# Optimization experiments

Measured on AMD Instinct MI355X. Metric: run time of the kernel, lower is better.

Reference implementation:

```python
import jax, jax.numpy as jnp
import numpy as np

B, S, D = 4, 4096, 768

def setup_inputs() -> dict:
    key = jax.random.key(0)
    kx, kq, kk, kv = jax.random.split(key, 4)
    x = jax.random.normal(kx, (B, S, D), dtype=jnp.float32)
    Wq = jax.random.normal(kq, (D, D), dtype=jnp.float32) * (D ** -0.5)
    Wk = jax.random.normal(kk, (D, D), dtype=jnp.float32) * (D ** -0.5)
    Wv = jax.random.normal(kv, (D, D), dtype=jnp.float32) * (D ** -0.5)
    return {"x": x, "Wq": Wq, "Wk": Wk, "Wv": Wv}

def reference(x, Wq, Wk, Wv):
    # q,k,v: [B,S,D]  (Linear with no bias)
    q = x @ Wq
    k = x @ Wk
    v = x @ Wv
    # full N x N causal score matrix, as in the original module
    scores = jnp.einsum('bqd,bkd->bqk', q, k)  # [B,S,S]
    seq = scores.shape[1]
    causal_mask = jnp.triu(jnp.ones((seq, seq), dtype=bool), k=1)  # True above diagonal
    scores = jnp.where(causal_mask[None, :, :], -jnp.inf, scores)
    scale = jnp.asarray(k.shape[-1], scores.dtype) ** 0.5
    weights = jax.nn.softmax(scores / scale, axis=-1)  # [B,S,S]
    # dropout p=0.0 -> identity (deterministic reference)
    context = jnp.einsum('bqk,bkd->bqd', weights, v)  # [B,S,D]
    return context
```

## Files before the change

### kernel.cpp

```cpp
#include <hip/hip_runtime.h>
#include <hip/hip_bf16.h>

typedef __attribute__((ext_vector_type(8))) _Float16 half8_t;
typedef __attribute__((ext_vector_type(4))) _Float16 half4_t;
typedef __attribute__((ext_vector_type(4))) float float4_t;

#define D_DIM 768
#define S_DIM 4096
#define B_DIM 4
#define M_DIM (B_DIM * S_DIM)
#define SD ((size_t)S_DIM * D_DIM)

#define GLOAD_LDS16(g, s)                                      \
  __builtin_amdgcn_global_load_lds(                            \
      (const __attribute__((address_space(1))) void*)(g),      \
      (__attribute__((address_space(3))) void*)(s), 16, 0, 0)

__device__ __forceinline__ float4_t mfma16(half8_t a, half8_t b, float4_t c) {
  return __builtin_amdgcn_mfma_f32_16x16x32_f16(a, b, c, 0, 0, 0);
}

__global__ __launch_bounds__(256) void prep_kernel(const float* __restrict__ x,
                                                   const float* __restrict__ W0,
                                                   const float* __restrict__ W1,
                                                   const float* __restrict__ W2,
                                                   _Float16* __restrict__ xh,
                                                   _Float16* __restrict__ WT) {
  __shared__ _Float16 tile[64][68];
  const int bid = blockIdx.x;
  if (bid < 12288) {
    int i = (bid * 256 + threadIdx.x) * 4;
    float4 v = *(const float4*)(x + i);
    half4_t o;
    o.x = (_Float16)v.x; o.y = (_Float16)v.y; o.z = (_Float16)v.z; o.w = (_Float16)v.w;
    *(half4_t*)(xh + i) = o;
  } else {
    int t = bid - 12288;
    int z = t / 144;
    int r = t % 144;
    int kx = r / 12, ny = r % 12;
    const float* W = (z == 0) ? W0 : (z == 1) ? W1 : W2;
    _Float16* o = WT + (size_t)z * D_DIM * D_DIM;
    int k0 = kx * 64, n0 = ny * 64;
#pragma unroll
    for (int i = 0; i < 16; ++i) {
      int idx = threadIdx.x + i * 256;
      int rr = idx >> 6, cc = idx & 63;
      tile[rr][cc] = (_Float16)W[(size_t)(k0 + rr) * D_DIM + n0 + cc];
    }
    __syncthreads();
#pragma unroll
    for (int i = 0; i < 16; ++i) {
      int idx = threadIdx.x + i * 256;
      int rr = idx >> 6, cc = idx & 63;
      o[(size_t)(n0 + rr) * D_DIM + k0 + cc] = tile[cc][rr];
    }
  }
}

template <bool SWAP>
__device__ __forceinline__ void core128(const _Float16* __restrict__ Ag,
                                        const _Float16* __restrict__ Bg,
                                        int lda, int ldb, int nt,
                                        char* lds, float4_t (&acc)[4][4]) {
  const int tid = threadIdx.x;
  const int w = tid >> 6, l = tid & 63;
  const int wr = w >> 1, wc = w & 1;
  const int l15 = l & 15, l4 = l >> 4;

  int sA[4], sB[4], sDst[4];
#pragma unroll
  for (int i = 0; i < 4; ++i) {
    int L = i * 256 + tid;
    int row = L >> 3, u = L & 7;
    int usw = u ^ (row & 7);
    sA[i] = row * lda + usw * 8;
    sB[i] = row * ldb + usw * 8;
    sDst[i] = (i * 256 + (tid & ~63)) * 16;
  }

  int aOff[2][4], bOff[2][4];
#pragma unroll
  for (int ks = 0; ks < 2; ++ks) {
#pragma unroll
    for (int i = 0; i < 4; ++i) {
      int ar = wr * 64 + i * 16 + l15;
      aOff[ks][i] = ar * 128 + (((ks * 4 + l4) ^ (ar & 7)) * 16);
      int br = wc * 64 + i * 16 + l15;
      bOff[ks][i] = 16384 + br * 128 + (((ks * 4 + l4) ^ (br & 7)) * 16);
    }
  }

#pragma unroll 1
  for (int kt = 0; kt < nt; ++kt) {
#pragma unroll
    for (int i = 0; i < 4; ++i)
      GLOAD_LDS16(Ag + (size_t)kt * 64 + sA[i], lds + sDst[i]);
#pragma unroll
    for (int i = 0; i < 4; ++i)
      GLOAD_LDS16(Bg + (size_t)kt * 64 + sB[i], lds + 16384 + sDst[i]);
    __syncthreads();
#pragma unroll
    for (int ks = 0; ks < 2; ++ks) {
      half8_t af[4], bf[4];
#pragma unroll
      for (int ni = 0; ni < 4; ++ni) bf[ni] = *(const half8_t*)(lds + bOff[ks][ni]);
#pragma unroll
      for (int mi = 0; mi < 4; ++mi) af[mi] = *(const half8_t*)(lds + aOff[ks][mi]);
      __builtin_amdgcn_s_setprio(1);
#pragma unroll
      for (int mi = 0; mi < 4; ++mi)
#pragma unroll
        for (int ni = 0; ni < 4; ++ni) {
          if (SWAP)
            acc[mi][ni] = mfma16(bf[ni], af[mi], acc[mi][ni]);
          else
            acc[mi][ni] = mfma16(af[mi], bf[ni], acc[mi][ni]);
        }
      __builtin_amdgcn_s_setprio(0);
    }
    __syncthreads();
  }
}

__global__ __launch_bounds__(256) void proj8_kernel(const _Float16* __restrict__ xh,
                                                    const _Float16* __restrict__ WT,
                                                    _Float16* __restrict__ qkv,
                                                    _Float16* __restrict__ vt) {
  __shared__ __align__(16) char lds[32768];
  const int bid = blockIdx.x;
  const int wid = (bid & 7) * 288 + (bid >> 3);
  const int rbg = wid / 18;
  const int rem = wid % 18;
  const int z = rem / 6;
  const int cb = rem % 6;

  const _Float16* Ag = xh + (size_t)rbg * 128 * D_DIM;
  const _Float16* Bg = WT + (size_t)z * D_DIM * D_DIM + (size_t)cb * 128 * D_DIM;
  float4_t acc[4][4];
#pragma unroll
  for (int a = 0; a < 4; ++a)
#pragma unroll
    for (int b = 0; b < 4; ++b) acc[a][b] = (float4_t){0.f, 0.f, 0.f, 0.f};

  const int tid = threadIdx.x;
  const int w = tid >> 6, l = tid & 63;
  const int wr = w >> 1, wc = w & 1;
  const int l15 = l & 15, l4 = l >> 4;

  if (z < 2) {
    core128<false>(Ag, Bg, D_DIM, D_DIM, 12, lds, acc);
    _Float16* C = qkv + (size_t)z * M_DIM * D_DIM;
#pragma unroll
    for (int mi = 0; mi < 4; ++mi)
#pragma unroll
      for (int ni = 0; ni < 4; ++ni) {
        int col = cb * 128 + wc * 64 + ni * 16 + l15;
#pragma unroll
        for (int j = 0; j < 4; ++j) {
          int row = rbg * 128 + wr * 64 + mi * 16 + l4 * 4 + j;
          C[(size_t)row * D_DIM + col] = (_Float16)acc[mi][ni][j];
        }
      }
  } else {
    core128<true>(Ag, Bg, D_DIM, D_DIM, 12, lds, acc);
#pragma unroll
    for (int mi = 0; mi < 4; ++mi) {
      int scol = rbg * 128 + wr * 64 + mi * 16 + l15;
      int bb = scol >> 12;
      int sl = scol & 4095;
      _Float16* vtb = vt + (size_t)bb * SD;
#pragma unroll
      for (int ni = 0; ni < 4; ++ni) {
#pragma unroll
        for (int j = 0; j < 4; ++j) {
          int drow = cb * 128 + wc * 64 + ni * 16 + l4 * 4 + j;
          vtb[(size_t)drow * S_DIM + sl] = (_Float16)acc[mi][ni][j];
        }
      }
    }
  }
}

__global__ __launch_bounds__(256) void gemm1_8_kernel(const _Float16* __restrict__ Q,
                                                      const _Float16* __restrict__ K,
                                                      _Float16* __restrict__ P,
                                                      float* __restrict__ rp) {
  __shared__ __align__(16) char lds[32768];
  const float SCALE = 0.036084391824351615f;
  const int bid = blockIdx.x;
  const int wid = (bid & 7) * 264 + (bid >> 3);
  const int z = wid / 528;
  const int t = wid % 528;
  int g = 0;
  while (g < 7 && (8 * (g + 1) * g + 10 * (g + 1)) <= t) ++g;
  int r = t - (8 * g * (g - 1) + 10 * g);
  int rbg, cb;
  if (r < 16 * g) {
    int cbg = r >> 4, wi = r & 15;
    rbg = 4 * g + (wi >> 2);
    cb = 4 * cbg + (wi & 3);
  } else {
    int r2 = r - 16 * g;
    const int ri[10] = {0, 1, 1, 2, 2, 2, 3, 3, 3, 3};
    const int rj[10] = {0, 0, 1, 0, 1, 2, 0, 1, 2, 3};
    rbg = 4 * g + ri[r2];
    cb = 4 * g + rj[r2];
  }

  const _Float16* Ag = Q + (size_t)z * SD + (size_t)rbg * 128 * D_DIM;
  const _Float16* Bg = K + (size_t)z * SD + (size_t)cb * 128 * D_DIM;
  float4_t acc[4][4];
#pragma unroll
  for (int a = 0; a < 4; ++a)
#pragma unroll
    for (int b = 0; b < 4; ++b) acc[a][b] = (float4_t){0.f, 0.f, 0.f, 0.f};
  core128<false>(Ag, Bg, D_DIM, D_DIM, 12, lds, acc);

  const int tid = threadIdx.x;
  const int w = tid >> 6, l = tid & 63;
  const int wr = w >> 1, wc = w & 1;
  const int l15 = l & 15, l4 = l >> 4;
  _Float16* Pz = P + (size_t)z * S_DIM * S_DIM;
  float* rpz = rp + (size_t)z * S_DIM * 64;
#pragma unroll
  for (int mi = 0; mi < 4; ++mi) {
#pragma unroll
    for (int j = 0; j < 4; ++j) {
      int row = rbg * 128 + wr * 64 + mi * 16 + l4 * 4 + j;
      float rs = 0.f;
#pragma unroll
      for (int ni = 0; ni < 4; ++ni) {
        int col = cb * 128 + wc * 64 + ni * 16 + l15;
        float v = (col <= row) ? __expf(acc[mi][ni][j] * SCALE - 4.0f) : 0.f;
        _Float16 ph = (_Float16)v;
        Pz[(size_t)row * S_DIM + col] = ph;
        rs += (float)ph;
      }
#pragma unroll
      for (int d = 1; d < 16; d <<= 1) rs += __shfl_xor(rs, d);
      if (l15 == 0) rpz[(size_t)row * 64 + cb * 2 + wc] = rs;
    }
  }
}

__global__ __launch_bounds__(256) void gemm2_8_kernel(const _Float16* __restrict__ P,
                                                      const _Float16* __restrict__ VT,
                                                      float* __restrict__ outp,
                                                      const float* __restrict__ rp) {
  __shared__ __align__(16) char lds[32768];
  __shared__ float rsm[128];
  const int bid = blockIdx.x;
  const int g = bid / 24;
  const int q = bid % 24;
  const int rbg = 31 - g;
  const int xcd = q & 7;
  const int slot = q >> 3;
  const int z = xcd >> 1;
  const int by = (xcd & 1) * 3 + slot;
  const int nt = 2 * (rbg + 1);

  const _Float16* Ag = P + (size_t)z * S_DIM * S_DIM + (size_t)rbg * 128 * S_DIM;
  const _Float16* Bg = VT + (size_t)z * SD + (size_t)by * 128 * S_DIM;
  float4_t acc[4][4];
#pragma unroll
  for (int a = 0; a < 4; ++a)
#pragma unroll
    for (int b = 0; b < 4; ++b) acc[a][b] = (float4_t){0.f, 0.f, 0.f, 0.f};
  core128<false>(Ag, Bg, S_DIM, S_DIM, nt, lds, acc);

  const int tid = threadIdx.x;
  if (tid < 128) {
    const float* p = rp + ((size_t)z * S_DIM + (size_t)rbg * 128 + tid) * 64;
    float s = 0.f;
    for (int i = 0; i < nt; ++i) s += p[i];
    rsm[tid] = 1.0f / s;
  }
  __syncthreads();

  const int w = tid >> 6, l = tid & 63;
  const int wr = w >> 1, wc = w & 1;
  const int l15 = l & 15, l4 = l >> 4;
#pragma unroll
  for (int mi = 0; mi < 4; ++mi) {
#pragma unroll
    for (int j = 0; j < 4; ++j) {
      int lrow = wr * 64 + mi * 16 + l4 * 4 + j;
      int row = rbg * 128 + lrow;
      float rinv = rsm[lrow];
#pragma unroll
      for (int ni = 0; ni < 4; ++ni) {
        int col = by * 128 + wc * 64 + ni * 16 + l15;
        outp[(size_t)z * SD + (size_t)row * D_DIM + col] = acc[mi][ni][j] * rinv;
      }
    }
  }
}

extern "C" void kernel_launch(void* const* d_in, const int* in_sizes, int n_in,
                              void* d_out, int out_size, void* d_ws, size_t ws_size,
                              hipStream_t stream) {
  const float* x = (const float*)d_in[0];
  const float* Wq = (const float*)d_in[1];
  const float* Wk = (const float*)d_in[2];
  const float* Wv = (const float*)d_in[3];
  float* out = (float*)d_out;
  char* ws = (char*)d_ws;

  const size_t XH_B = (size_t)M_DIM * D_DIM * 2;
  const size_t QKV_B = 3 * XH_B;
  const size_t VT_B = XH_B;
  const size_t WT_B = (size_t)3 * D_DIM * D_DIM * 2;
  const size_t BASE_END = XH_B + QKV_B + VT_B + WT_B;

  _Float16* xh = (_Float16*)ws;
  _Float16* qkv = (_Float16*)(ws + XH_B);
  _Float16* Q = qkv;
  _Float16* K = qkv + (size_t)M_DIM * D_DIM;
  _Float16* vt = (_Float16*)(ws + XH_B + QKV_B);
  _Float16* wt = (_Float16*)(ws + XH_B + QKV_B + VT_B);

  float* rp = (float*)(ws + BASE_END);
  _Float16* P = (_Float16*)(ws + BASE_END + (size_t)4259840);

  prep_kernel<<<dim3(12720), dim3(256), 0, stream>>>(x, Wq, Wk, Wv, xh, wt);
  proj8_kernel<<<dim3(2304), dim3(256), 0, stream>>>(xh, wt, qkv, vt);
  gemm1_8_kernel<<<dim3(2112), dim3(256), 0, stream>>>(Q, K, P, rp);
  gemm2_8_kernel<<<dim3(768), dim3(256), 0, stream>>>(P, vt, out, rp);
}
```

Measured before the change: 264.4 us.

## Double-buffer GEMM core with async LDS prefetch and 32-wide K tiles

The shared GEMM core now uses two 16KB LDS buffers with K-tiles of 32 instead of one 32KB buffer with K-tiles of 64. The next tile is prefetched via global_load_lds while the current one feeds MFMAs, synchronized with explicit vmcnt waits and raw barriers. This is meant to hide global-load latency behind compute. The cost is twice as many iterations and barriers, each doing half the MFMA work, plus a new swizzle for the narrower rows. Callers' tile counts are doubled, and the row-sum loop keeps its old count.

```diff
diff --git a/kernel.cpp b/kernel.cpp
--- a/kernel.cpp
+++ b/kernel.cpp
@@ -68,59 +68,71 @@
   const int wr = w >> 1, wc = w & 1;
   const int l15 = l & 15, l4 = l >> 4;
 
-  int sA[4], sB[4], sDst[4];
+  int aS[2], bS[2], dstL[2];
+#pragma unroll
+  for (int i = 0; i < 2; ++i) {
+    int g = i * 256 + tid;
+    int row = g >> 2, u = g & 3;
+    int usw = (u ^ ((row >> 1) & 3)) * 8;
+    aS[i] = row * lda + usw;
+    bS[i] = row * ldb + usw;
+    dstL[i] = (i * 256 + (tid & ~63)) * 16;
+  }
+
+  int aOff[4], bOff[4];
 #pragma unroll
   for (int i = 0; i < 4; ++i) {
-    int L = i * 256 + tid;
-    int row = L >> 3, u = L & 7;
-    int usw = u ^ (row & 7);
-    sA[i] = row * lda + usw * 8;
-    sB[i] = row * ldb + usw * 8;
-    sDst[i] = (i * 256 + (tid & ~63)) * 16;
-  }
-
-  int aOff[2][4], bOff[2][4];
-#pragma unroll
-  for (int ks = 0; ks < 2; ++ks) {
-#pragma unroll
-    for (int i = 0; i < 4; ++i) {
-      int ar = wr * 64 + i * 16 + l15;
-      aOff[ks][i] = ar * 128 + (((ks * 4 + l4) ^ (ar & 7)) * 16);
-      int br = wc * 64 + i * 16 + l15;
-      bOff[ks][i] = 16384 + br * 128 + (((ks * 4 + l4) ^ (br & 7)) * 16);
-    }
-  }
+    int ar = wr * 64 + i * 16 + l15;
+    aOff[i] = ar * 64 + ((l4 ^ ((ar >> 1) & 3)) * 16);
+    int br = wc * 64 + i * 16 + l15;
+    bOff[i] = 8192 + br * 64 + ((l4 ^ ((br >> 1) & 3)) * 16);
+  }
+
+#define STG(kt)                                                               \
+  do {                                                                        \
+    char* s = lds + ((kt) & 1) * 16384;                                       \
+    const _Float16* As = Ag + (size_t)(kt) * 32;                              \
+    const _Float16* Bs = Bg + (size_t)(kt) * 32;                              \
+    GLOAD_LDS16(As + aS[0], s + dstL[0]);                                     \
+    GLOAD_LDS16(As + aS[1], s + dstL[1]);                                     \
+    GLOAD_LDS16(Bs + bS[0], s + 8192 + dstL[0]);                              \
+    GLOAD_LDS16(Bs + bS[1], s + 8192 + dstL[1]);                              \
+  } while (0)
+
+  STG(0);
 
 #pragma unroll 1
   for (int kt = 0; kt < nt; ++kt) {
-#pragma unroll
-    for (int i = 0; i < 4; ++i)
-      GLOAD_LDS16(Ag + (size_t)kt * 64 + sA[i], lds + sDst[i]);
-#pragma unroll
-    for (int i = 0; i < 4; ++i)
-      GLOAD_LDS16(Bg + (size_t)kt * 64 + sB[i], lds + 16384 + sDst[i]);
-    __syncthreads();
-#pragma unroll
-    for (int ks = 0; ks < 2; ++ks) {
-      half8_t af[4], bf[4];
-#pragma unroll
-      for (int ni = 0; ni < 4; ++ni) bf[ni] = *(const half8_t*)(lds + bOff[ks][ni]);
-#pragma unroll
-      for (int mi = 0; mi < 4; ++mi) af[mi] = *(const half8_t*)(lds + aOff[ks][mi]);
-      __builtin_amdgcn_s_setprio(1);
-#pragma unroll
-      for (int mi = 0; mi < 4; ++mi)
-#pragma unroll
-        for (int ni = 0; ni < 4; ++ni) {
-          if (SWAP)
-            acc[mi][ni] = mfma16(bf[ni], af[mi], acc[mi][ni]);
-          else
-            acc[mi][ni] = mfma16(af[mi], bf[ni], acc[mi][ni]);
-        }
-      __builtin_amdgcn_s_setprio(0);
-    }
-    __syncthreads();
-  }
+    __builtin_amdgcn_s_barrier();
+    if (kt + 1 < nt) STG(kt + 1);
+    __builtin_amdgcn_sched_barrier(0);
+    if (kt + 1 < nt)
+      asm volatile("s_waitcnt vmcnt(4)" ::: "memory");
+    else
+      asm volatile("s_waitcnt vmcnt(0)" ::: "memory");
+    __builtin_amdgcn_sched_barrier(0);
+    __builtin_amdgcn_s_barrier();
+    __builtin_amdgcn_sched_barrier(0);
+
+    const char* s = lds + (kt & 1) * 16384;
+    half8_t af[4], bf[4];
+#pragma unroll
+    for (int ni = 0; ni < 4; ++ni) bf[ni] = *(const half8_t*)(s + bOff[ni]);
+#pragma unroll
+    for (int mi = 0; mi < 4; ++mi) af[mi] = *(const half8_t*)(s + aOff[mi]);
+    __builtin_amdgcn_s_setprio(1);
+#pragma unroll
+    for (int mi = 0; mi < 4; ++mi)
+#pragma unroll
+      for (int ni = 0; ni < 4; ++ni) {
+        if (SWAP)
+          acc[mi][ni] = mfma16(bf[ni], af[mi], acc[mi][ni]);
+        else
+          acc[mi][ni] = mfma16(af[mi], bf[ni], acc[mi][ni]);
+      }
+    __builtin_amdgcn_s_setprio(0);
+  }
+#undef STG
 }
 
 __global__ __launch_bounds__(256) void proj8_kernel(const _Float16* __restrict__ xh,
@@ -149,7 +161,7 @@
   const int l15 = l & 15, l4 = l >> 4;
 
   if (z < 2) {
-    core128<false>(Ag, Bg, D_DIM, D_DIM, 12, lds, acc);
+    core128<false>(Ag, Bg, D_DIM, D_DIM, 24, lds, acc);
     _Float16* C = qkv + (size_t)z * M_DIM * D_DIM;
 #pragma unroll
     for (int mi = 0; mi < 4; ++mi)
@@ -163,7 +175,7 @@
         }
       }
   } else {
-    core128<true>(Ag, Bg, D_DIM, D_DIM, 12, lds, acc);
+    core128<true>(Ag, Bg, D_DIM, D_DIM, 24, lds, acc);
 #pragma unroll
     for (int mi = 0; mi < 4; ++mi) {
       int scol = rbg * 128 + wr * 64 + mi * 16 + l15;
@@ -215,7 +227,7 @@
   for (int a = 0; a < 4; ++a)
 #pragma unroll
     for (int b = 0; b < 4; ++b) acc[a][b] = (float4_t){0.f, 0.f, 0.f, 0.f};
-  core128<false>(Ag, Bg, D_DIM, D_DIM, 12, lds, acc);
+  core128<false>(Ag, Bg, D_DIM, D_DIM, 24, lds, acc);
 
   const int tid = threadIdx.x;
   const int w = tid >> 6, l = tid & 63;
@@ -258,7 +270,7 @@
   const int slot = q >> 3;
   const int z = xcd >> 1;
   const int by = (xcd & 1) * 3 + slot;
-  const int nt = 2 * (rbg + 1);
+  const int nt = 4 * (rbg + 1);
 
   const _Float16* Ag = P + (size_t)z * S_DIM * S_DIM + (size_t)rbg * 128 * S_DIM;
   const _Float16* Bg = VT + (size_t)z * SD + (size_t)by * 128 * S_DIM;
@@ -273,7 +285,8 @@
   if (tid < 128) {
     const float* p = rp + ((size_t)z * S_DIM + (size_t)rbg * 128 + tid) * 64;
     float s = 0.f;
-    for (int i = 0; i < nt; ++i) s += p[i];
+    const int np = 2 * (rbg + 1);
+    for (int i = 0; i < np; ++i) s += p[i];
     rsm[tid] = 1.0f / s;
   }
   __syncthreads();
```

After: 269.1 us. About the same (+1.8%).
